# Kernel tuning notes

Measured on AMD Instinct MI355X. Metric: run time of the kernel, lower is better.

Reference implementation:

```python
import jax, jax.numpy as jnp
import numpy as np

B, L, D, H, FF = 2, 512, 512, 8, 2048
LP1 = L + 1
HD = D // H
RFF_DIM, RB_HID = 32, 64
EPS = 1e-5


def _layernorm(x, g, b):
    mu = jnp.mean(x, axis=-1, keepdims=True)
    var = jnp.mean(jnp.square(x - mu), axis=-1, keepdims=True)
    return (x - mu) * jax.lax.rsqrt(var + EPS) * g + b


def setup_inputs() -> dict:
    key = jax.random.key(0)
    ks = jax.random.split(key, 12)
    def w(k, shape, scale=0.02):
        return jax.random.normal(k, shape, jnp.float32) * scale
    return {
        "x": jax.random.normal(ks[0], (B, LP1, D), jnp.float32),
        "s_norm": jax.random.uniform(ks[1], (B, L), jnp.float32),
        # fixed random-fourier-feature frequencies (requires_grad=False in torch)
        "rff": jax.random.normal(ks[2], (1, RFF_DIM), jnp.float32) * 2.0,
        # rel-bias MLP: Linear(32,64) -> GELU -> Linear(64,nhead), torch (out,in) layout
        "rb_w1": w(ks[3], (RB_HID, RFF_DIM)), "rb_b1": jnp.zeros(RB_HID, jnp.float32),
        "rb_w2": w(ks[4], (H, RB_HID)), "rb_b2": jnp.zeros(H, jnp.float32),
        "n1_g": jnp.ones(D, jnp.float32), "n1_b": jnp.zeros(D, jnp.float32),
        "n2_g": jnp.ones(D, jnp.float32), "n2_b": jnp.zeros(D, jnp.float32),
        # MHA packed qkv in-projection and out-projection
        "in_w": w(ks[5], (3 * D, D)), "in_b": jnp.zeros(3 * D, jnp.float32),
        "out_w": w(ks[6], (D, D)), "out_b": jnp.zeros(D, jnp.float32),
        # FF: Linear(D,FF) -> GELU -> Linear(FF,D)
        "ff_w1": w(ks[7], (FF, D)), "ff_b1": jnp.zeros(FF, jnp.float32),
        "ff_w2": w(ks[8], (D, FF)), "ff_b2": jnp.zeros(D, jnp.float32),
    }


def reference(x, s_norm, rff, rb_w1, rb_b1, rb_w2, rb_b2,
              n1_g, n1_b, n2_g, n2_b, in_w, in_b, out_w, out_b,
              ff_w1, ff_b1, ff_w2, ff_b2):
    b = x.shape[0]
    # s_full: prepend zero for the extra (e.g. CLS) position -> (B, L+1)
    s_full = jnp.concatenate([jnp.zeros((b, 1), x.dtype), s_norm], axis=1)
    # pairwise deltas -> RFF sin features -> 2-layer MLP -> per-head bias
    ds = s_full[:, :, None] - s_full[:, None, :]              # (B, L+1, L+1)
    feat = jnp.sin(ds[..., None] * rff[0])                    # (B, L+1, L+1, 32)
    hid = jax.nn.gelu(feat @ rb_w1.T + rb_b1, approximate=False)
    bias = hid @ rb_w2.T + rb_b2                              # (B, L+1, L+1, H)
    bias = jnp.transpose(bias, (0, 3, 1, 2))                  # (B, H, L+1, L+1)

    # pre-LN self-attention
    z = _layernorm(x, n1_g, n1_b)
    qkv = z @ in_w.T + in_b                                   # (B, L+1, 3D)
    q, k, v = jnp.split(qkv, 3, axis=-1)
    def heads(t):
        return jnp.transpose(t.reshape(b, LP1, H, HD), (0, 2, 1, 3))
    q, k, v = heads(q), heads(k), heads(v)                    # (B, H, L+1, HD)
    scores = jnp.einsum("bhqd,bhkd->bhqk", q, k) / np.sqrt(HD) + bias
    attn = jax.nn.softmax(scores, axis=-1)
    a = jnp.einsum("bhqk,bhkd->bhqd", attn, v)                # (B, H, L+1, HD)
    a = jnp.transpose(a, (0, 2, 1, 3)).reshape(b, LP1, D)
    a = a @ out_w.T + out_b
    x = x + a

    # pre-LN feed-forward
    h2 = _layernorm(x, n2_g, n2_b)
    ffo = jax.nn.gelu(h2 @ ff_w1.T + ff_b1, approximate=False) @ ff_w2.T + ff_b2
    return x + ffo
```

## Files before the change

kernel.cpp:

```cpp
#include <hip/hip_runtime.h>
#include <hip/hip_bf16.h>
#include <math.h>

constexpr int B_   = 2;
constexpr int L_   = 512;
constexpr int LP1  = 513;
constexpr int D_   = 512;
constexpr int H_   = 8;
constexpr int HD_  = 64;
constexpr int FF_  = 2048;
constexpr int RFFD = 32;
constexpr int RBH  = 64;
constexpr int M_   = B_ * LP1;
constexpr float EPS_ = 1e-5f;
constexpr int NT_  = 8193;
constexpr int QB_  = 2;
constexpr int QBLKS_ = (LP1 + QB_ - 1) / QB_;

constexpr size_t OFFZ   = 0;
constexpr size_t OFFX1  = OFFZ  + (size_t)M_ * D_;
constexpr size_t OFFQKV = OFFX1 + (size_t)M_ * D_;
constexpr size_t OFFKT  = OFFQKV + (size_t)M_ * 3 * D_;
constexpr size_t OFFA   = OFFKT + (size_t)B_ * D_ * LP1;
constexpr size_t OFFT   = OFFA + (size_t)M_ * D_;

typedef __attribute__((ext_vector_type(4))) float f32x4;
typedef __attribute__((ext_vector_type(8))) __bf16 bf16x8;
typedef __attribute__((ext_vector_type(4))) __bf16 bf16x4;

__device__ __forceinline__ float gelu_exact(float x) {
    return 0.5f * x * (1.0f + erff(x * 0.70710678118654752f));
}

__device__ __forceinline__ __bf16 f2b(float f) {
    union { float f; unsigned u; } a; a.f = f;
    const unsigned r = (a.u + 0x7FFFu + ((a.u >> 16) & 1u)) >> 16;
    union { unsigned short s; __bf16 b; } o; o.s = (unsigned short)r;
    return o.b;
}

__global__ void k_btab(const float* __restrict__ rff, const float* __restrict__ w1,
                       const float* __restrict__ b1, const float* __restrict__ w2,
                       const float* __restrict__ b2, float* __restrict__ table) {
    const int idx = blockIdx.x * 256 + threadIdx.x;
    if (idx >= NT_) return;
    const float ds = (float)idx * (2.0f / (NT_ - 1)) - 1.0f;
    float feat[RFFD];
    #pragma unroll
    for (int k = 0; k < RFFD; ++k) feat[k] = sinf(ds * rff[k]);
    float bh[H_];
    #pragma unroll
    for (int h = 0; h < H_; ++h) bh[h] = b2[h];
    for (int l = 0; l < RBH; ++l) {
        float acc = b1[l];
        #pragma unroll
        for (int k = 0; k < RFFD; ++k) acc += feat[k] * w1[l * RFFD + k];
        const float gl = gelu_exact(acc);
        #pragma unroll
        for (int h = 0; h < H_; ++h) bh[h] += gl * w2[h * RBH + l];
    }
    #pragma unroll
    for (int h = 0; h < H_; ++h) table[(size_t)idx * H_ + h] = bh[h];
}

__global__ void k_ln(const float* __restrict__ x, const float* __restrict__ g,
                     const float* __restrict__ be, float* __restrict__ out) {
    const int m = blockIdx.x;
    const int t = threadIdx.x;
    __shared__ float red[256];
    const float v0 = x[(size_t)m * D_ + t];
    const float v1 = x[(size_t)m * D_ + t + 256];
    red[t] = v0 + v1;
    __syncthreads();
    for (int off = 128; off > 0; off >>= 1) {
        if (t < off) red[t] += red[t + off];
        __syncthreads();
    }
    const float mu = red[0] * (1.0f / D_);
    __syncthreads();
    const float d0 = v0 - mu, d1 = v1 - mu;
    red[t] = d0 * d0 + d1 * d1;
    __syncthreads();
    for (int off = 128; off > 0; off >>= 1) {
        if (t < off) red[t] += red[t + off];
        __syncthreads();
    }
    const float rstd = rsqrtf(red[0] * (1.0f / D_) + EPS_);
    out[(size_t)m * D_ + t]       = d0 * rstd * g[t]       + be[t];
    out[(size_t)m * D_ + t + 256] = d1 * rstd * g[t + 256] + be[t + 256];
}

template <int ACT, bool RES, int BM>
__global__ __launch_bounds__(256)
void k_gemm_mfma(const float* __restrict__ A, const float* __restrict__ W,
                 const float* __restrict__ bias, const float* __restrict__ res,
                 float* __restrict__ C, int M, int N, int K) {
    constexpr int BN = 64, BK = 32, PAD = 8;
    constexpr int LA = (BM * BK) / (4 * 256);
    constexpr int WRT = 2;
    constexpr int WCT = (BM == 64) ? 2 : 1;
    __shared__ __bf16 As[2][BM][BK + PAD];
    __shared__ __bf16 Bs[2][BN][BK + PAD];
    const int t = threadIdx.x;

    const int nx = N / BN;
    int bid = blockIdx.x;
    {
        const int nb = gridDim.x;
        const int q = nb >> 3, r = nb & 7;
        const int xc = bid & 7, o = bid >> 3;
        bid = (xc < r ? xc * (q + 1) : r * (q + 1) + (xc - r) * q) + o;
    }
    const int m0 = (bid / nx) * BM;
    const int n0 = (bid % nx) * BN;

    const int wid  = t >> 6;
    const int lane = t & 63;
    const int wr   = (BM == 64) ? ((wid >> 1) * 32) : 0;
    const int wc   = (BM == 64) ? ((wid & 1) * 32) : (wid * 16);
    const int fr   = lane & 15;
    const int kg   = lane >> 4;
    const int lrow = t >> 3;
    const int lf4  = t & 7;

    f32x4 acc[WRT][WCT] = {};
    float4 pa[LA], pw[2];
    const int nk = K / BK;

    auto load_tile = [&](int kt) {
        const int kbase = kt * BK + lf4 * 4;
        #pragma unroll
        for (int i = 0; i < LA; ++i) {
            const int gm = m0 + lrow + i * 32;
            pa[i] = make_float4(0.f, 0.f, 0.f, 0.f);
            if (gm < M) pa[i] = *(const float4*)&A[(size_t)gm * K + kbase];
        }
        #pragma unroll
        for (int i = 0; i < 2; ++i)
            pw[i] = *(const float4*)&W[(size_t)(n0 + lrow + i * 32) * K + kbase];
    };
    auto store_tile = [&](int buf) {
        #pragma unroll
        for (int i = 0; i < LA; ++i) {
            bf16x4 v;
            v[0] = f2b(pa[i].x); v[1] = f2b(pa[i].y);
            v[2] = f2b(pa[i].z); v[3] = f2b(pa[i].w);
            *(bf16x4*)&As[buf][lrow + i * 32][lf4 * 4] = v;
        }
        #pragma unroll
        for (int i = 0; i < 2; ++i) {
            bf16x4 v;
            v[0] = f2b(pw[i].x); v[1] = f2b(pw[i].y);
            v[2] = f2b(pw[i].z); v[3] = f2b(pw[i].w);
            *(bf16x4*)&Bs[buf][lrow + i * 32][lf4 * 4] = v;
        }
    };

    load_tile(0);
    store_tile(0);
    __syncthreads();
    int cur = 0;
    for (int kt = 0; kt < nk; ++kt) {
        if (kt + 1 < nk) load_tile(kt + 1);
        bf16x8 af[WRT], bfr[WCT];
        #pragma unroll
        for (int i2 = 0; i2 < WRT; ++i2)
            af[i2] = *(const bf16x8*)&As[cur][wr + i2 * 16 + fr][kg * 8];
        #pragma unroll
        for (int j2 = 0; j2 < WCT; ++j2)
            bfr[j2] = *(const bf16x8*)&Bs[cur][wc + j2 * 16 + fr][kg * 8];
        #pragma unroll
        for (int i2 = 0; i2 < WRT; ++i2)
            #pragma unroll
            for (int j2 = 0; j2 < WCT; ++j2)
                acc[i2][j2] = __builtin_amdgcn_mfma_f32_16x16x32_bf16(
                    af[i2], bfr[j2], acc[i2][j2], 0, 0, 0);
        if (kt + 1 < nk) store_tile(cur ^ 1);
        __syncthreads();
        cur ^= 1;
    }

    #pragma unroll
    for (int ti = 0; ti < WRT; ++ti) {
        #pragma unroll
        for (int tj = 0; tj < WCT; ++tj) {
            const int gn = n0 + wc + tj * 16 + fr;
            const float bv = bias[gn];
            #pragma unroll
            for (int v = 0; v < 4; ++v) {
                const int gm = m0 + wr + ti * 16 + kg * 4 + v;
                if (gm < M) {
                    float val = acc[ti][tj][v] + bv;
                    if (ACT == 1) val = gelu_exact(val);
                    if (RES) val += res[(size_t)gm * N + gn];
                    C[(size_t)gm * N + gn] = val;
                }
            }
        }
    }
}

__global__ void k_kT(const float* __restrict__ qkv, float* __restrict__ kT) {
    __shared__ float tile[32][33];
    const int b  = blockIdx.z;
    const int j0 = blockIdx.x * 32;
    const int d0 = blockIdx.y * 32;
    const int tx = threadIdx.x;
    const int ty = threadIdx.y;
    #pragma unroll
    for (int q = 0; q < 4; ++q) {
        const int j = j0 + ty + q * 8;
        if (j < LP1)
            tile[ty + q * 8][tx] = qkv[((size_t)(b * LP1 + j)) * (3 * D_) + D_ + d0 + tx];
    }
    __syncthreads();
    #pragma unroll
    for (int q = 0; q < 4; ++q) {
        const int j = j0 + tx;
        const int d = d0 + ty + q * 8;
        if (j < LP1)
            kT[((size_t)b * D_ + d) * LP1 + j] = tile[tx][ty + q * 8];
    }
}

__global__ __launch_bounds__(256)
void k_attn(const float* __restrict__ qkv, const float* __restrict__ kT,
            const float* __restrict__ s_norm, const float* __restrict__ table,
            float* __restrict__ a) {
    const int b   = blockIdx.x / QBLKS_;
    const int qi0 = (blockIdx.x % QBLKS_) * QB_;
    const int t = threadIdx.x;
    __shared__ float q_s[QB_][D_];
    __shared__ float s_s[LP1 + 1];
    __shared__ float p_s[QB_][H_][LP1 + 3];

    for (int idx = t; idx < QB_ * D_; idx += 256) {
        const int q = idx >> 9;
        const int d = idx & 511;
        const int i = min(qi0 + q, LP1 - 1);
        q_s[q][d] = qkv[(size_t)(b * LP1 + i) * (3 * D_) + d];
    }
    for (int j = t; j < LP1; j += 256)
        s_s[j] = (j == 0) ? 0.f : s_norm[b * L_ + j - 1];
    __syncthreads();

    const int g  = t >> 5;
    const int sl = t & 31;
    constexpr int NJ = 17;

    float s_i[QB_];
    #pragma unroll
    for (int q = 0; q < QB_; ++q) s_i[q] = s_s[min(qi0 + q, LP1 - 1)];

    float acc[QB_][NJ] = {};
    const float* kTg = kT + ((size_t)b * D_ + g * HD_) * LP1;
    for (int dd = 0; dd < HD_; ++dd) {
        const float* row = kTg + (size_t)dd * LP1;
        float qv[QB_];
        #pragma unroll
        for (int q = 0; q < QB_; ++q) qv[q] = q_s[q][g * HD_ + dd];
        #pragma unroll
        for (int jj = 0; jj < NJ; ++jj) {
            const int j = sl + jj * 32;
            const float kv = (j < LP1) ? row[j] : 0.f;
            #pragma unroll
            for (int q = 0; q < QB_; ++q) acc[q][jj] = fmaf(qv[q], kv, acc[q][jj]);
        }
    }

    #pragma unroll
    for (int q = 0; q < QB_; ++q) {
        float mx = -1e30f;
        #pragma unroll
        for (int jj = 0; jj < NJ; ++jj) {
            const int j = sl + jj * 32;
            if (j < LP1) {
                const float ds = s_i[q] - s_s[j];
                float u = (ds + 1.0f) * ((NT_ - 1) * 0.5f);
                u = fminf(fmaxf(u, 0.0f), (float)(NT_ - 2));
                const int i0 = (int)u;
                const float f = u - (float)i0;
                const float b0  = table[(size_t)i0 * H_ + g];
                const float b1v = table[(size_t)(i0 + 1) * H_ + g];
                acc[q][jj] = b0 + f * (b1v - b0) + 0.125f * acc[q][jj];
                mx = fmaxf(mx, acc[q][jj]);
            }
        }
        #pragma unroll
        for (int off = 16; off > 0; off >>= 1) mx = fmaxf(mx, __shfl_xor(mx, off, 32));
        float sum = 0.f;
        #pragma unroll
        for (int jj = 0; jj < NJ; ++jj) {
            const int j = sl + jj * 32;
            if (j < LP1) {
                acc[q][jj] = __expf(acc[q][jj] - mx);
                sum += acc[q][jj];
            }
        }
        #pragma unroll
        for (int off = 16; off > 0; off >>= 1) sum += __shfl_xor(sum, off, 32);
        const float inv = 1.0f / sum;
        #pragma unroll
        for (int jj = 0; jj < NJ; ++jj) {
            const int j = sl + jj * 32;
            if (j < LP1) p_s[q][g][j] = acc[q][jj] * inv;
        }
    }
    __syncthreads();

    const float* vbase = qkv + (size_t)(b * LP1) * (3 * D_) + 2 * D_;
    for (int e = t; e < D_; e += 256) {
        const int h = e >> 6;
        float o00 = 0.f, o01 = 0.f, o10 = 0.f, o11 = 0.f;
        int j = 0;
        for (; j + 2 <= LP1; j += 2) {
            const float v0 = vbase[(size_t)(j + 0) * (3 * D_) + e];
            const float v1 = vbase[(size_t)(j + 1) * (3 * D_) + e];
            o00 = fmaf(p_s[0][h][j + 0], v0, o00);
            o01 = fmaf(p_s[0][h][j + 1], v1, o01);
            o10 = fmaf(p_s[1][h][j + 0], v0, o10);
            o11 = fmaf(p_s[1][h][j + 1], v1, o11);
        }
        for (; j < LP1; ++j) {
            const float v0 = vbase[(size_t)j * (3 * D_) + e];
            o00 = fmaf(p_s[0][h][j], v0, o00);
            o10 = fmaf(p_s[1][h][j], v0, o10);
        }
        if (qi0 < LP1)
            a[(size_t)(b * LP1 + qi0) * D_ + e] = o00 + o01;
        if (qi0 + 1 < LP1)
            a[(size_t)(b * LP1 + qi0 + 1) * D_ + e] = o10 + o11;
    }
}

extern "C" void kernel_launch(void* const* d_in, const int* in_sizes, int n_in,
                              void* d_out, int out_size, void* d_ws, size_t ws_size,
                              hipStream_t stream) {
    const float* x      = (const float*)d_in[0];
    const float* s_norm = (const float*)d_in[1];
    const float* rff    = (const float*)d_in[2];
    const float* rb_w1  = (const float*)d_in[3];
    const float* rb_b1  = (const float*)d_in[4];
    const float* rb_w2  = (const float*)d_in[5];
    const float* rb_b2  = (const float*)d_in[6];
    const float* n1_g   = (const float*)d_in[7];
    const float* n1_b   = (const float*)d_in[8];
    const float* n2_g   = (const float*)d_in[9];
    const float* n2_b   = (const float*)d_in[10];
    const float* in_w   = (const float*)d_in[11];
    const float* in_b   = (const float*)d_in[12];
    const float* out_w  = (const float*)d_in[13];
    const float* out_b  = (const float*)d_in[14];
    const float* ff_w1  = (const float*)d_in[15];
    const float* ff_b1  = (const float*)d_in[16];
    const float* ff_w2  = (const float*)d_in[17];
    const float* ff_b2  = (const float*)d_in[18];

    float* ws    = (float*)d_ws;
    float* z     = ws + OFFZ;
    float* x1    = ws + OFFX1;
    float* qkv   = ws + OFFQKV;
    float* kT    = ws + OFFKT;
    float* a     = ws + OFFA;
    float* table = ws + OFFT;
    float* h2    = z;
    float* hact  = qkv;

    k_btab<<<(NT_ + 255) / 256, 256, 0, stream>>>(rff, rb_w1, rb_b1, rb_w2, rb_b2, table);
    k_ln<<<M_, 256, 0, stream>>>(x, n1_g, n1_b, z);
    k_gemm_mfma<0, false, 64><<<(3 * D_ / 64) * ((M_ + 63) / 64), 256, 0, stream>>>(
        z, in_w, in_b, nullptr, qkv, M_, 3 * D_, D_);
    k_kT<<<dim3((LP1 + 31) / 32, D_ / 32, B_), dim3(32, 8), 0, stream>>>(qkv, kT);
    k_attn<<<B_ * QBLKS_, 256, 0, stream>>>(qkv, kT, s_norm, table, a);
    k_gemm_mfma<0, true, 32><<<(D_ / 64) * ((M_ + 31) / 32), 256, 0, stream>>>(
        a, out_w, out_b, x, x1, M_, D_, D_);
    k_ln<<<M_, 256, 0, stream>>>(x1, n2_g, n2_b, h2);
    k_gemm_mfma<1, false, 64><<<(FF_ / 64) * ((M_ + 63) / 64), 256, 0, stream>>>(
        h2, ff_w1, ff_b1, nullptr, hact, M_, FF_, D_);
    k_gemm_mfma<0, true, 32><<<(D_ / 64) * ((M_ + 31) / 32), 256, 0, stream>>>(
        hact, ff_w2, ff_b2, x1, (float*)d_out, M_, D_, FF_);
}
```

Before: 299.2 us.

## Pre-convert weights to bf16, store FF hidden in bf16, split attention by head halves

Adds a kernel that converts all GEMM weights to bf16 once per call, so the GEMMs load bf16 weight tiles directly instead of converting fp32 on every tile load. The FF1 GEMM now writes its GELU output in bf16 and FF2 reads bf16 A tiles, halving that intermediate's traffic. Attention blocks now cover 4 query rows and half the heads each, giving more blocks and more reuse of each V load. The cost is four extra conversion launches per call and extra workspace.

```diff
diff --git a/kernel.cpp b/kernel.cpp
--- a/kernel.cpp
+++ b/kernel.cpp
@@ -14,8 +14,8 @@
 constexpr int M_   = B_ * LP1;
 constexpr float EPS_ = 1e-5f;
 constexpr int NT_  = 8193;
-constexpr int QB_  = 2;
-constexpr int QBLKS_ = (LP1 + QB_ - 1) / QB_;
+constexpr int QB_  = 4;
+constexpr int QT_  = (LP1 + QB_ - 1) / QB_;
 
 constexpr size_t OFFZ   = 0;
 constexpr size_t OFFX1  = OFFZ  + (size_t)M_ * D_;
@@ -23,6 +23,7 @@
 constexpr size_t OFFKT  = OFFQKV + (size_t)M_ * 3 * D_;
 constexpr size_t OFFA   = OFFKT + (size_t)B_ * D_ * LP1;
 constexpr size_t OFFT   = OFFA + (size_t)M_ * D_;
+constexpr size_t OFFWB  = OFFT + (size_t)NT_ * H_;
 
 typedef __attribute__((ext_vector_type(4))) float f32x4;
 typedef __attribute__((ext_vector_type(8))) __bf16 bf16x8;
@@ -37,6 +38,23 @@
     const unsigned r = (a.u + 0x7FFFu + ((a.u >> 16) & 1u)) >> 16;
     union { unsigned short s; __bf16 b; } o; o.s = (unsigned short)r;
     return o.b;
+}
+
+__device__ __forceinline__ bf16x8 bzero8() {
+    bf16x8 v;
+    #pragma unroll
+    for (int i = 0; i < 8; ++i) v[i] = (__bf16)0.0f;
+    return v;
+}
+
+__global__ void k_w2b(const float* __restrict__ src, __bf16* __restrict__ dst, int n) {
+    const int i = (blockIdx.x * 256 + threadIdx.x) * 4;
+    if (i < n) {
+        const float4 v = *(const float4*)&src[i];
+        bf16x4 o;
+        o[0] = f2b(v.x); o[1] = f2b(v.y); o[2] = f2b(v.z); o[3] = f2b(v.w);
+        *(bf16x4*)&dst[i] = o;
+    }
 }
 
 __global__ void k_btab(const float* __restrict__ rff, const float* __restrict__ w1,
@@ -90,12 +108,13 @@
     out[(size_t)m * D_ + t + 256] = d1 * rstd * g[t + 256] + be[t + 256];
 }
 
-template <int ACT, bool RES, int BM>
+template <int ACT, bool RES, int BM, typename AT, typename OT>
 __global__ __launch_bounds__(256)
-void k_gemm_mfma(const float* __restrict__ A, const float* __restrict__ W,
+void k_gemm_mfma(const AT* __restrict__ A, const __bf16* __restrict__ W,
                  const float* __restrict__ bias, const float* __restrict__ res,
-                 float* __restrict__ C, int M, int N, int K) {
+                 OT* __restrict__ C, int M, int N, int K) {
     constexpr int BN = 64, BK = 32, PAD = 8;
+    constexpr bool ABF = (sizeof(AT) == 2);
     constexpr int LA = (BM * BK) / (4 * 256);
     constexpr int WRT = 2;
     constexpr int WCT = (BM == 64) ? 2 : 1;
@@ -120,39 +139,52 @@
     const int wc   = (BM == 64) ? ((wid & 1) * 32) : (wid * 16);
     const int fr   = lane & 15;
     const int kg   = lane >> 4;
-    const int lrow = t >> 3;
-    const int lf4  = t & 7;
 
     f32x4 acc[WRT][WCT] = {};
-    float4 pa[LA], pw[2];
+    float4 pa[LA > 0 ? LA : 1];
+    bf16x8 pab, pwb;
     const int nk = K / BK;
 
     auto load_tile = [&](int kt) {
-        const int kbase = kt * BK + lf4 * 4;
-        #pragma unroll
-        for (int i = 0; i < LA; ++i) {
-            const int gm = m0 + lrow + i * 32;
-            pa[i] = make_float4(0.f, 0.f, 0.f, 0.f);
-            if (gm < M) pa[i] = *(const float4*)&A[(size_t)gm * K + kbase];
-        }
-        #pragma unroll
-        for (int i = 0; i < 2; ++i)
-            pw[i] = *(const float4*)&W[(size_t)(n0 + lrow + i * 32) * K + kbase];
+        const int kb = kt * BK;
+        if constexpr (!ABF) {
+            const int lrow = t >> 3, lf4 = t & 7;
+            #pragma unroll
+            for (int i = 0; i < LA; ++i) {
+                const int gm = m0 + lrow + i * 32;
+                pa[i] = make_float4(0.f, 0.f, 0.f, 0.f);
+                if (gm < M) pa[i] = *(const float4*)&A[(size_t)gm * K + kb + lf4 * 4];
+            }
+        } else {
+            const int lrow = t >> 2, lkc = t & 3;
+            if (BM == 64 || t < 128) {
+                const int gm = m0 + lrow;
+                pab = (gm < M) ? *(const bf16x8*)&A[(size_t)gm * K + kb + lkc * 8]
+                               : bzero8();
+            }
+        }
+        {
+            const int lrow = t >> 2, lkc = t & 3;
+            pwb = *(const bf16x8*)&W[(size_t)(n0 + lrow) * K + kb + lkc * 8];
+        }
     };
     auto store_tile = [&](int buf) {
-        #pragma unroll
-        for (int i = 0; i < LA; ++i) {
-            bf16x4 v;
-            v[0] = f2b(pa[i].x); v[1] = f2b(pa[i].y);
-            v[2] = f2b(pa[i].z); v[3] = f2b(pa[i].w);
-            *(bf16x4*)&As[buf][lrow + i * 32][lf4 * 4] = v;
-        }
-        #pragma unroll
-        for (int i = 0; i < 2; ++i) {
-            bf16x4 v;
-            v[0] = f2b(pw[i].x); v[1] = f2b(pw[i].y);
-            v[2] = f2b(pw[i].z); v[3] = f2b(pw[i].w);
-            *(bf16x4*)&Bs[buf][lrow + i * 32][lf4 * 4] = v;
+        if constexpr (!ABF) {
+            const int lrow = t >> 3, lf4 = t & 7;
+            #pragma unroll
+            for (int i = 0; i < LA; ++i) {
+                bf16x4 v;
+                v[0] = f2b(pa[i].x); v[1] = f2b(pa[i].y);
+                v[2] = f2b(pa[i].z); v[3] = f2b(pa[i].w);
+                *(bf16x4*)&As[buf][lrow + i * 32][lf4 * 4] = v;
+            }
+        } else {
+            const int lrow = t >> 2, lkc = t & 3;
+            if (BM == 64 || t < 128) *(bf16x8*)&As[buf][lrow][lkc * 8] = pab;
+        }
+        {
+            const int lrow = t >> 2, lkc = t & 3;
+            *(bf16x8*)&Bs[buf][lrow][lkc * 8] = pwb;
         }
     };
 
@@ -193,7 +225,8 @@
                     float val = acc[ti][tj][v] + bv;
                     if (ACT == 1) val = gelu_exact(val);
                     if (RES) val += res[(size_t)gm * N + gn];
-                    C[(size_t)gm * N + gn] = val;
+                    if constexpr (sizeof(OT) == 2) C[(size_t)gm * N + gn] = f2b(val);
+                    else                           C[(size_t)gm * N + gn] = val;
                 }
             }
         }
@@ -227,63 +260,69 @@
 void k_attn(const float* __restrict__ qkv, const float* __restrict__ kT,
             const float* __restrict__ s_norm, const float* __restrict__ table,
             float* __restrict__ a) {
-    const int b   = blockIdx.x / QBLKS_;
-    const int qi0 = (blockIdx.x % QBLKS_) * QB_;
+    const int hh  = blockIdx.x & 1;
+    const int qt  = (blockIdx.x >> 1) % QT_;
+    const int b   = blockIdx.x / (2 * QT_);
+    const int qi0 = qt * QB_;
     const int t = threadIdx.x;
-    __shared__ float q_s[QB_][D_];
+    __shared__ float q_s[QB_][256];
     __shared__ float s_s[LP1 + 1];
-    __shared__ float p_s[QB_][H_][LP1 + 3];
-
-    for (int idx = t; idx < QB_ * D_; idx += 256) {
-        const int q = idx >> 9;
-        const int d = idx & 511;
+    __shared__ float p_s[QB_][4][LP1 + 3];
+
+    for (int idx = t; idx < QB_ * 256; idx += 256) {
+        const int q = idx >> 8;
+        const int dl = idx & 255;
         const int i = min(qi0 + q, LP1 - 1);
-        q_s[q][d] = qkv[(size_t)(b * LP1 + i) * (3 * D_) + d];
+        q_s[q][dl] = qkv[(size_t)(b * LP1 + i) * (3 * D_) + hh * 256 + dl];
     }
     for (int j = t; j < LP1; j += 256)
         s_s[j] = (j == 0) ? 0.f : s_norm[b * L_ + j - 1];
     __syncthreads();
 
-    const int g  = t >> 5;
-    const int sl = t & 31;
+    const int g   = t >> 5;
+    const int sl  = t & 31;
+    const int hl  = g >> 1;
+    const int hid = hh * 4 + hl;
+    const int qp  = g & 1;
     constexpr int NJ = 17;
 
-    float s_i[QB_];
-    #pragma unroll
-    for (int q = 0; q < QB_; ++q) s_i[q] = s_s[min(qi0 + q, LP1 - 1)];
-
-    float acc[QB_][NJ] = {};
-    const float* kTg = kT + ((size_t)b * D_ + g * HD_) * LP1;
+    float s_i[2];
+    #pragma unroll
+    for (int q2 = 0; q2 < 2; ++q2)
+        s_i[q2] = s_s[min(qi0 + qp * 2 + q2, LP1 - 1)];
+
+    float acc[2][NJ] = {};
+    const float* kTg = kT + ((size_t)b * D_ + hid * HD_) * LP1;
     for (int dd = 0; dd < HD_; ++dd) {
         const float* row = kTg + (size_t)dd * LP1;
-        float qv[QB_];
-        #pragma unroll
-        for (int q = 0; q < QB_; ++q) qv[q] = q_s[q][g * HD_ + dd];
+        float qv[2];
+        #pragma unroll
+        for (int q2 = 0; q2 < 2; ++q2) qv[q2] = q_s[qp * 2 + q2][hl * 64 + dd];
         #pragma unroll
         for (int jj = 0; jj < NJ; ++jj) {
             const int j = sl + jj * 32;
             const float kv = (j < LP1) ? row[j] : 0.f;
             #pragma unroll
-            for (int q = 0; q < QB_; ++q) acc[q][jj] = fmaf(qv[q], kv, acc[q][jj]);
-        }
-    }
-
-    #pragma unroll
-    for (int q = 0; q < QB_; ++q) {
+            for (int q2 = 0; q2 < 2; ++q2) acc[q2][jj] = fmaf(qv[q2], kv, acc[q2][jj]);
+        }
+    }
+
+    #pragma unroll
+    for (int q2 = 0; q2 < 2; ++q2) {
         float mx = -1e30f;
         #pragma unroll
         for (int jj = 0; jj < NJ; ++jj) {
             const int j = sl + jj * 32;
             if (j < LP1) {
-                const float ds = s_i[q] - s_s[j];
+                const float ds = s_i[q2] - s_s[j];
                 float u = (ds + 1.0f) * ((NT_ - 1) * 0.5f);
                 u = fminf(fmaxf(u, 0.0f), (float)(NT_ - 2));
                 const int i0 = (int)u;
                 const float f = u - (float)i0;
-                const float b0  = table[(size_t)i0 * H_ + g];
-                const float b1v = table[(size_t)(i0 + 1) * H_ + g];
-                acc[q][jj] = b0 + f * (b1v - b0) + 0.125f * acc[q][jj];
-                mx = fmaxf(mx, acc[q][jj]);
+                const float b0  = table[(size_t)i0 * H_ + hid];
+                const float b1v = table[(size_t)(i0 + 1) * H_ + hid];
+                acc[q2][jj] = b0 + f * (b1v - b0) + 0.125f * acc[q2][jj];
+                mx = fmaxf(mx, acc[q2][jj]);
             }
         }
         #pragma unroll
@@ -293,8 +332,8 @@
         for (int jj = 0; jj < NJ; ++jj) {
             const int j = sl + jj * 32;
             if (j < LP1) {
-                acc[q][jj] = __expf(acc[q][jj] - mx);
-                sum += acc[q][jj];
+                acc[q2][jj] = __expf(acc[q2][jj] - mx);
+                sum += acc[q2][jj];
             }
         }
         #pragma unroll
@@ -303,33 +342,35 @@
         #pragma unroll
         for (int jj = 0; jj < NJ; ++jj) {
             const int j = sl + jj * 32;
-            if (j < LP1) p_s[q][g][j] = acc[q][jj] * inv;
-        }
-    }
-    __syncthreads();
-
-    const float* vbase = qkv + (size_t)(b * LP1) * (3 * D_) + 2 * D_;
-    for (int e = t; e < D_; e += 256) {
-        const int h = e >> 6;
-        float o00 = 0.f, o01 = 0.f, o10 = 0.f, o11 = 0.f;
-        int j = 0;
-        for (; j + 2 <= LP1; j += 2) {
-            const float v0 = vbase[(size_t)(j + 0) * (3 * D_) + e];
-            const float v1 = vbase[(size_t)(j + 1) * (3 * D_) + e];
-            o00 = fmaf(p_s[0][h][j + 0], v0, o00);
-            o01 = fmaf(p_s[0][h][j + 1], v1, o01);
-            o10 = fmaf(p_s[1][h][j + 0], v0, o10);
-            o11 = fmaf(p_s[1][h][j + 1], v1, o11);
-        }
-        for (; j < LP1; ++j) {
-            const float v0 = vbase[(size_t)j * (3 * D_) + e];
-            o00 = fmaf(p_s[0][h][j], v0, o00);
-            o10 = fmaf(p_s[1][h][j], v0, o10);
-        }
-        if (qi0 < LP1)
-            a[(size_t)(b * LP1 + qi0) * D_ + e] = o00 + o01;
-        if (qi0 + 1 < LP1)
-            a[(size_t)(b * LP1 + qi0 + 1) * D_ + e] = o10 + o11;
+            if (j < LP1) p_s[qp * 2 + q2][hl][j] = acc[q2][jj] * inv;
+        }
+    }
+    __syncthreads();
+
+    const int hl2 = t >> 6;
+    const float* vbase = qkv + (size_t)(b * LP1) * (3 * D_) + 2 * D_ + hh * 256;
+    float o0 = 0.f, o1 = 0.f, o2 = 0.f, o3 = 0.f;
+    int j = 0;
+    for (; j + 2 <= LP1; j += 2) {
+        const float v0 = vbase[(size_t)(j + 0) * (3 * D_) + t];
+        const float v1 = vbase[(size_t)(j + 1) * (3 * D_) + t];
+        o0 = fmaf(p_s[0][hl2][j], v0, o0); o0 = fmaf(p_s[0][hl2][j + 1], v1, o0);
+        o1 = fmaf(p_s[1][hl2][j], v0, o1); o1 = fmaf(p_s[1][hl2][j + 1], v1, o1);
+        o2 = fmaf(p_s[2][hl2][j], v0, o2); o2 = fmaf(p_s[2][hl2][j + 1], v1, o2);
+        o3 = fmaf(p_s[3][hl2][j], v0, o3); o3 = fmaf(p_s[3][hl2][j + 1], v1, o3);
+    }
+    for (; j < LP1; ++j) {
+        const float v0 = vbase[(size_t)j * (3 * D_) + t];
+        o0 = fmaf(p_s[0][hl2][j], v0, o0);
+        o1 = fmaf(p_s[1][hl2][j], v0, o1);
+        o2 = fmaf(p_s[2][hl2][j], v0, o2);
+        o3 = fmaf(p_s[3][hl2][j], v0, o3);
+    }
+    const float oq[4] = {o0, o1, o2, o3};
+    #pragma unroll
+    for (int q = 0; q < QB_; ++q) {
+        const int i = qi0 + q;
+        if (i < LP1) a[(size_t)(b * LP1 + i) * D_ + hh * 256 + t] = oq[q];
     }
 }
 
@@ -364,19 +405,33 @@
     float* a     = ws + OFFA;
     float* table = ws + OFFT;
     float* h2    = z;
-    float* hact  = qkv;
-
+    __bf16* hactb = (__bf16*)qkv;
+
+    __bf16* wb      = (__bf16*)(ws + OFFWB);
+    __bf16* in_wb   = wb;
+    __bf16* out_wb  = in_wb  + (size_t)3 * D_ * D_;
+    __bf16* ff_w1b  = out_wb + (size_t)D_ * D_;
+    __bf16* ff_w2b  = ff_w1b + (size_t)FF_ * D_;
+
+    k_w2b<<<(3 * D_ * D_ / 4 + 255) / 256, 256, 0, stream>>>(in_w, in_wb, 3 * D_ * D_);
+    k_w2b<<<(D_ * D_ / 4 + 255) / 256, 256, 0, stream>>>(out_w, out_wb, D_ * D_);
+    k_w2b<<<(FF_ * D_ / 4 + 255) / 256, 256, 0, stream>>>(ff_w1, ff_w1b, FF_ * D_);
+    k_w2b<<<(D_ * FF_ / 4 + 255) / 256, 256, 0, stream>>>(ff_w2, ff_w2b, D_ * FF_);
     k_btab<<<(NT_ + 255) / 256, 256, 0, stream>>>(rff, rb_w1, rb_b1, rb_w2, rb_b2, table);
     k_ln<<<M_, 256, 0, stream>>>(x, n1_g, n1_b, z);
-    k_gemm_mfma<0, false, 64><<<(3 * D_ / 64) * ((M_ + 63) / 64), 256, 0, stream>>>(
-        z, in_w, in_b, nullptr, qkv, M_, 3 * D_, D_);
+    k_gemm_mfma<0, false, 64, float, float>
+        <<<(3 * D_ / 64) * ((M_ + 63) / 64), 256, 0, stream>>>(
+        z, in_wb, in_b, nullptr, qkv, M_, 3 * D_, D_);
     k_kT<<<dim3((LP1 + 31) / 32, D_ / 32, B_), dim3(32, 8), 0, stream>>>(qkv, kT);
-    k_attn<<<B_ * QBLKS_, 256, 0, stream>>>(qkv, kT, s_norm, table, a);
-    k_gemm_mfma<0, true, 32><<<(D_ / 64) * ((M_ + 31) / 32), 256, 0, stream>>>(
-        a, out_w, out_b, x, x1, M_, D_, D_);
+    k_attn<<<B_ * QT_ * 2, 256, 0, stream>>>(qkv, kT, s_norm, table, a);
+    k_gemm_mfma<0, true, 32, float, float>
+        <<<(D_ / 64) * ((M_ + 31) / 32), 256, 0, stream>>>(
+        a, out_wb, out_b, x, x1, M_, D_, D_);
     k_ln<<<M_, 256, 0, stream>>>(x1, n2_g, n2_b, h2);
-    k_gemm_mfma<1, false, 64><<<(FF_ / 64) * ((M_ + 63) / 64), 256, 0, stream>>>(
-        h2, ff_w1, ff_b1, nullptr, hact, M_, FF_, D_);
-    k_gemm_mfma<0, true, 32><<<(D_ / 64) * ((M_ + 31) / 32), 256, 0, stream>>>(
-        hact, ff_w2, ff_b2, x1, (float*)d_out, M_, D_, FF_);
-}
+    k_gemm_mfma<1, false, 64, float, __bf16>
+        <<<(FF_ / 64) * ((M_ + 63) / 64), 256, 0, stream>>>(
+        h2, ff_w1b, ff_b1, nullptr, hactb, M_, FF_, D_);
+    k_gemm_mfma<0, true, 32, __bf16, float>
+        <<<(D_ / 64) * ((M_ + 31) / 32), 256, 0, stream>>>(
+        hactb, ff_w2b, ff_b2, x1, (float*)d_out, M_, D_, FF_);
+}
```

Result: faster. 293.0 us (-2.1%).
